# Optimization experiments

Measured on AMD Instinct MI355X. Metric: run time of the kernel, lower is better.

## Reference

```python
import jax, jax.numpy as jnp
import numpy as np

# Geometry constants (LinearProbeGeom)
N_DET = 128
N_T = 2048
DT_S = 2.5e-08        # 40 MHz sampling
PITCH_M = 3.0e-04
C_M_S = 1540.0
NX, NY = 256, 256
X0_M, DX_M = -0.0192, 1.5e-04
Y0_M, DY_M = 1.0e-03, 1.5e-04
ARRAY_X0_M, ARRAY_Y_M = -0.0192, 0.0
N_FFT = N_T  # fft_pad = 0
EPS = np.float32(np.finfo(np.float32).eps)


def _constants():
    freq = np.fft.rfftfreq(N_FFT, d=DT_S)
    omega = (2.0 * np.pi * freq).astype(np.float32)            # (F,)
    fw = np.ones_like(omega)
    if omega.size > 2:
        fw[1:-1] = 2.0
    if N_FFT % 2 == 0 and omega.size > 1:
        fw[-1] = 1.0
    kx = (2.0 * np.pi * np.fft.fftfreq(N_DET, d=PITCH_M)).astype(np.float32)  # (D,)
    xs = (X0_M + np.arange(NX) * DX_M - ARRAY_X0_M).astype(np.float32)        # (X,)
    ys = (Y0_M + np.arange(NY) * DY_M - ARRAY_Y_M).astype(np.float32)         # (Y,)
    # Hann apodization over detectors (buffer, non-trainable)
    apod = (0.5 - 0.5 * np.cos(2.0 * np.pi * np.arange(N_DET) / max(N_DET - 1, 1))).astype(np.float32)
    return (jnp.asarray(omega), jnp.asarray(fw), jnp.asarray(kx),
            jnp.asarray(xs), jnp.asarray(ys), jnp.asarray(apod))


def setup_inputs() -> dict:
    key = jax.random.key(0)
    sino = jax.random.normal(key, (8, 1, N_DET, N_T), dtype=jnp.float32)
    return {"sino": sino}


def reference(sino):
    omega, fw, kx, xs, ys, apod = _constants()
    B, C, D, T = sino.shape
    # per-(B,C) standardization over (det, time)
    mean = jnp.mean(sino, axis=(-1, -2), keepdims=True)
    sn = sino - mean
    var = jnp.mean(sn * sn, axis=(-1, -2), keepdims=True)
    sn = sn / jnp.sqrt(var + EPS)
    # time window is rectangular (window=None) -> identity
    sw = sn * apod[None, None, :, None]
    # 2D spectrum: rfft over time, fft over detectors
    spec = jnp.fft.rfft(sw, n=N_FFT, axis=-1)          # (B,C,D,F)
    spec = jnp.fft.fft(spec, axis=2)                   # (B,C,D,F)
    # Stolt dispersion: kz^2 = (w/c)^2 - kx^2, clamped
    kz_sq = (omega / C_M_S)[None, :] ** 2 - (kx ** 2)[:, None]   # (D,F)
    kz = jnp.sqrt(jnp.maximum(kz_sq, 0.0))
    prop_mask = (kz_sq > 0.0).astype(jnp.float32)
    # fold propagation mask and frequency weighting into the spectrum
    sf = spec * (prop_mask * fw[None, :])[None, None, :, :]      # (B,C,D,F) complex
    # per-depth phase shift and frequency reduction
    phase_y = jnp.exp(1j * kz[None, :, :] * ys[:, None, None])   # (Y,D,F) complex64
    band = jnp.einsum('bcdf,ydf->bcyd', sf, phase_y)             # (B,C,Y,D)
    # lateral inverse transform via explicit phase matrix
    phase_x = jnp.exp(1j * kx[:, None] * xs[None, :])            # (D,X)
    img = jnp.einsum('bcyd,dx->bcyx', band, phase_x)             # (B,C,Y,X)
    img_mag = jnp.abs(img)
    apod_sum = jnp.maximum(jnp.sum(apod), EPS)
    fw_sum = jnp.maximum(jnp.sum(fw), EPS)
    return img_mag / (apod_sum * fw_sum)
```

## Files before the change

kernel.cpp:

```cpp
#include <hip/hip_runtime.h>
#include <math.h>

#define NB 8
#define ND 128
#define NT 2048
#define NF 1025
#define NYY 256
#define NXX 256

#define SPEC_BYTES 8396800
#define BAND_PART_BYTES 2097152
#define BANDH_PART_BYTES 1048576
#define ROWSTAT_OFF 0
#define SPECT_OFF  8192
#define SF_OFF     (SPECT_OFF + SPEC_BYTES)
#define BAND_OFF   (SF_OFF + SPEC_BYTES)

__global__ __launch_bounds__(256) void fk_tfft(const float* __restrict__ sino,
                                               float2* __restrict__ specT,
                                               float2* __restrict__ rowstat) {
  const int row = blockIdx.x;
  const int d = row & (ND - 1);
  const int tid = threadIdx.x;
  __shared__ float2 bufA[1024];
  __shared__ float2 bufB[1024];
  __shared__ float2 wsum[4];
  const float ap = (float)(0.5 - 0.5 * cos(6.283185307179586 * (double)d / 127.0));
  const float2* in = (const float2*)(sino + (size_t)row * NT);
  float s = 0.f, q = 0.f;
  for (int i = tid; i < 1024; i += 256) {
    float2 v = in[i];
    s += v.x + v.y;
    q += v.x * v.x + v.y * v.y;
    bufA[i] = make_float2(v.x * ap, v.y * ap);
  }
  #pragma unroll
  for (int o = 32; o > 0; o >>= 1) {
    s += __shfl_down(s, o);
    q += __shfl_down(q, o);
  }
  if ((tid & 63) == 0) wsum[tid >> 6] = make_float2(s, q);
  __syncthreads();
  if (tid == 0) {
    rowstat[row] = make_float2(wsum[0].x + wsum[1].x + wsum[2].x + wsum[3].x,
                               wsum[0].y + wsum[1].y + wsum[2].y + wsum[3].y);
  }
  float2* src = bufA;
  float2* dst = bufB;
  for (int p = 1; p <= 512; p <<= 1) {
    #pragma unroll
    for (int it = 0; it < 2; ++it) {
      int i = tid + it * 256;
      int k = i & (p - 1);
      float2 u = src[i];
      float2 v = src[i + 512];
      float ang = -3.14159265358979323846f * ((float)k / (float)p);
      float sn, cs; __sincosf(ang, &sn, &cs);
      float2 vw = make_float2(v.x * cs - v.y * sn, v.x * sn + v.y * cs);
      int j = ((i - k) << 1) + k;
      dst[j]     = make_float2(u.x + vw.x, u.y + vw.y);
      dst[j + p] = make_float2(u.x - vw.x, u.y - vw.y);
    }
    __syncthreads();
    float2* t = src; src = dst; dst = t;
  }
  float2* out = specT + (size_t)row * NF;
  for (int k = tid; k < 1024; k += 256) {
    float2 zk = src[k];
    float2 zc = src[(1024 - k) & 1023]; zc.y = -zc.y;
    float2 xe = make_float2(0.5f * (zk.x + zc.x), 0.5f * (zk.y + zc.y));
    float ax = zk.x - zc.x, ay = zk.y - zc.y;
    float2 xo = make_float2(0.5f * ay, -0.5f * ax);
    float ang = -3.14159265358979323846f * ((float)k / 1024.0f);
    float sn, cs; __sincosf(ang, &sn, &cs);
    out[k] = make_float2(xe.x + cs * xo.x - sn * xo.y,
                         xe.y + cs * xo.y + sn * xo.x);
  }
  if (tid == 0) {
    float2 z0 = src[0];
    out[1024] = make_float2(z0.x - z0.y, 0.0f);
  }
}

__global__ __launch_bounds__(256) void fk_dfft(const float2* __restrict__ specT,
                                               float2* __restrict__ sf) {
  const int b = blockIdx.y;
  const int f0 = blockIdx.x * 4;
  const int sub = threadIdx.x >> 6;
  const int i = threadIdx.x & 63;
  const int f = f0 + sub;
  const bool valid = (f < NF);
  __shared__ float2 A[4][128];
  __shared__ float2 Bf[4][128];
  if (valid) {
    const float2* col = specT + ((size_t)b * ND) * NF + f;
    A[sub][i]      = col[(size_t)i * NF];
    A[sub][i + 64] = col[(size_t)(i + 64) * NF];
  }
  __syncthreads();
  float2 (*src)[128] = A;
  float2 (*dst)[128] = Bf;
  for (int p = 1; p <= 64; p <<= 1) {
    if (valid) {
      int k = i & (p - 1);
      float2 u = src[sub][i];
      float2 v = src[sub][i + 64];
      float ang = -3.14159265358979323846f * ((float)k / (float)p);
      float sn, cs; __sincosf(ang, &sn, &cs);
      float2 vw = make_float2(v.x * cs - v.y * sn, v.x * sn + v.y * cs);
      int j = ((i - k) << 1) + k;
      dst[sub][j]     = make_float2(u.x + vw.x, u.y + vw.y);
      dst[sub][j + p] = make_float2(u.x - vw.x, u.y - vw.y);
    }
    __syncthreads();
    float2 (*t)[128] = src; src = dst; dst = t;
  }
  if (valid) {
    const float fwv = (f == 0 || f == NF - 1) ? 1.0f : 2.0f;
    double freqd = (double)f / 5.12e-5;
    float omega = (float)(freqd * 6.283185307179586);
    float woc = omega / 1540.0f;
    float woc2 = __fmul_rn(woc, woc);
    #pragma unroll
    for (int h = 0; h < 2; ++h) {
      int kd = i + h * 64;
      int kt = kd < 64 ? kd : kd - 128;
      float kxv = (float)(6.283185307179586 * ((double)kt / 0.0384));
      float kzsq = __fsub_rn(woc2, __fmul_rn(kxv, kxv));
      float m = (kzsq > 0.0f) ? fwv : 0.0f;
      float2 v = src[sub][kd];
      sf[((size_t)(b * ND + kd)) * NF + f] = make_float2(v.x * m, v.y * m);
    }
  }
}

__device__ __forceinline__ unsigned int bf16rne(float x) {
  unsigned int u = __float_as_uint(x);
  return (u + 0x7fffu + ((u >> 16) & 1u)) >> 16;
}

__global__ __launch_bounds__(256, 3) void fk_band(const float2* __restrict__ sf,
                                                  unsigned int* __restrict__ bandh,
                                                  int flen_base, int fpad) {
  const int dblk = blockIdx.x;
  const int part = blockIdx.y;
  const int f0 = part * flen_base;
  const int flen = min(flen_base, NF - f0);
  const int tid = threadIdx.x;
  const int w = tid >> 6, l = tid & 63;
  const int d = dblk * 4 + w;

  extern __shared__ float lds[];
  float2* sfs = (float2*)lds;
  float4* kcs = (float4*)(lds + 64 * fpad);

  {
    const int row = tid >> 3;
    const int wr = row >> 3, br = row & 7;
    const int dr = dblk * 4 + wr;
    const float2* srcp = sf + ((size_t)(br * ND + dr)) * NF + f0;
    for (int ff = tid & 7; ff < fpad; ff += 8)
      sfs[row * fpad + ff] = (ff < flen) ? srcp[ff] : make_float2(0.f, 0.f);
  }
  for (int e = tid; e < 4 * fpad; e += 256) {
    const int wk = e / fpad, ff = e - wk * fpad;
    float kzv = 0.f;
    if (ff < flen) {
      int dk = dblk * 4 + wk;
      int kt = dk < 64 ? dk : dk - 128;
      float kxv = (float)(6.283185307179586 * ((double)kt / 0.0384));
      float kx2 = __fmul_rn(kxv, kxv);
      int f = f0 + ff;
      double freqd = (double)f / 5.12e-5;
      float omega = (float)(freqd * 6.283185307179586);
      float woc = omega / 1540.0f;
      float kzsq = __fsub_rn(__fmul_rn(woc, woc), kx2);
      kzv = (kzsq > 0.0f) ? sqrtf(kzsq) : 0.0f;
    }
    float sd, cd;
    __sincosf(kzv * 1.5e-4f, &sd, &cd);
    kcs[e] = make_float4(kzv, cd, sd, 0.f);
  }
  __syncthreads();

  const float y0 = (float)(1.0e-3 + (double)(4 * l) * 1.5e-4);

  float2 acc[8][4];
  #pragma unroll
  for (int b = 0; b < 8; ++b)
    #pragma unroll
    for (int i = 0; i < 4; ++i) acc[b][i] = make_float2(0.f, 0.f);

  const float4* kcw = kcs + w * fpad;
  const float2* rows = sfs + (w * 8) * fpad;

  #pragma unroll 2
  for (int ff = 0; ff < fpad; ++ff) {
    const float4 k4 = kcw[ff];
    float s0, c0;
    __sincosf(k4.x * y0, &s0, &c0);
    float2 ph[4];
    ph[0] = make_float2(c0, s0);
    #pragma unroll
    for (int i = 0; i < 3; ++i)
      ph[i + 1] = make_float2(ph[i].x * k4.y - ph[i].y * k4.z,
                              ph[i].x * k4.z + ph[i].y * k4.y);
    #pragma unroll
    for (int b = 0; b < 8; ++b) {
      float2 p = rows[b * fpad + ff];
      #pragma unroll
      for (int i = 0; i < 4; ++i) {
        acc[b][i].x = fmaf(p.x, ph[i].x, fmaf(-p.y, ph[i].y, acc[b][i].x));
        acc[b][i].y = fmaf(p.x, ph[i].y, fmaf( p.y, ph[i].x, acc[b][i].y));
      }
    }
  }

  unsigned int* outp = bandh + (size_t)part * (NB * ND * NYY);
  #pragma unroll
  for (int b = 0; b < 8; ++b) {
    uint4 pk;
    pk.x = bf16rne(acc[b][0].x) | (bf16rne(acc[b][0].y) << 16);
    pk.y = bf16rne(acc[b][1].x) | (bf16rne(acc[b][1].y) << 16);
    pk.z = bf16rne(acc[b][2].x) | (bf16rne(acc[b][2].y) << 16);
    pk.w = bf16rne(acc[b][3].x) | (bf16rne(acc[b][3].y) << 16);
    ((uint4*)(outp + ((size_t)(b * ND + d)) * NYY))[l] = pk;
  }
}

__global__ __launch_bounds__(256) void fk_sum(const unsigned int* __restrict__ bandh,
                                              float2* __restrict__ bandS, int nparts) {
  const int n = blockIdx.x * 256 + threadIdx.x;
  float sx = 0.f, sy = 0.f;
  for (int p = 0; p < nparts; ++p) {
    unsigned int u = bandh[(size_t)p * (NB * ND * NYY) + n];
    sx += __uint_as_float(u << 16);
    sy += __uint_as_float(u & 0xffff0000u);
  }
  bandS[n] = make_float2(sx, sy);
}

__global__ __launch_bounds__(256) void fk_img(const float2* __restrict__ bandS,
                                              const float2* __restrict__ rowstat,
                                              float* __restrict__ out, float inv_norm) {
  const int y = blockIdx.x;
  const int b = blockIdx.y;
  const int tid = threadIdx.x;
  __shared__ float2 A[256];
  __shared__ float2 Bb[256];
  __shared__ float2 spart[2];
  float2 myrs = make_float2(0.f, 0.f);
  if (tid < 128) myrs = rowstat[b * ND + tid];
  {
    float2 v = make_float2(0.f, 0.f);
    if (tid < 64)        v = bandS[((size_t)(b * ND + tid)) * NYY + y];
    else if (tid >= 192) v = bandS[((size_t)(b * ND + tid - 128)) * NYY + y];
    A[tid] = v;
  }
  {
    float s = myrs.x, q = myrs.y;
    #pragma unroll
    for (int o = 32; o > 0; o >>= 1) {
      s += __shfl_down(s, o);
      q += __shfl_down(q, o);
    }
    if (tid < 128 && (tid & 63) == 0) spart[tid >> 6] = make_float2(s, q);
  }
  __syncthreads();
  const float nInv = 1.0f / 262144.0f;
  float ssum = spart[0].x + spart[1].x;
  float qsum = spart[0].y + spart[1].y;
  float mean = ssum * nInv;
  float var = qsum * nInv - mean * mean;
  float scl = 1.0f / sqrtf(var + 1.1920928955078125e-7f);

  float2* src = A;
  float2* dst = Bb;
  for (int p = 1; p <= 128; p <<= 1) {
    if (tid < 128) {
      int i = tid;
      int k = i & (p - 1);
      float2 u = src[i];
      float2 v = src[i + 128];
      float ang = 3.14159265358979323846f * ((float)k / (float)p);
      float sn, cs; __sincosf(ang, &sn, &cs);
      float2 vw = make_float2(v.x * cs - v.y * sn, v.x * sn + v.y * cs);
      int j = ((i - k) << 1) + k;
      dst[j]     = make_float2(u.x + vw.x, u.y + vw.y);
      dst[j + p] = make_float2(u.x - vw.x, u.y - vw.y);
    }
    __syncthreads();
    float2* t = src; src = dst; dst = t;
  }
  float2 r = src[tid];
  float mag = sqrtf(r.x * r.x + r.y * r.y);
  out[((size_t)b * NYY + y) * NXX + tid] = mag * scl * inv_norm;
}

extern "C" void kernel_launch(void* const* d_in, const int* in_sizes, int n_in,
                              void* d_out, int out_size, void* d_ws, size_t ws_size,
                              hipStream_t stream) {
  const float* sino = (const float*)d_in[0];
  float* out = (float*)d_out;
  char* ws = (char*)d_ws;

  float2*       rowstat = (float2*)(ws + ROWSTAT_OFF);
  float2*       specT   = (float2*)(ws + SPECT_OFF);
  float2*       sf      = (float2*)(ws + SF_OFF);
  unsigned int* bandh   = (unsigned int*)(ws + BAND_OFF);

  int FPART = 8;
  if (ws_size >= (size_t)BAND_OFF + 24u * BANDH_PART_BYTES + BAND_PART_BYTES) FPART = 24;
  const int flen_base = (NF + FPART - 1) / FPART;
  const int fpad = (flen_base + 1) & ~1;
  const size_t band_lds = (size_t)fpad * 320;
  float2* bandS = (float2*)(ws + BAND_OFF + (size_t)FPART * BANDH_PART_BYTES);

  double apod_sum = 0.0;
  for (int n = 0; n < ND; ++n) apod_sum += 0.5 - 0.5 * cos(6.283185307179586 * (double)n / 127.0);
  const float inv_norm = (float)(1.0 / (apod_sum * 2048.0));

  fk_tfft<<<NB * ND, 256, 0, stream>>>(sino, specT, rowstat);
  fk_dfft<<<dim3((NF + 3) / 4, NB), 256, 0, stream>>>(specT, sf);
  fk_band<<<dim3(32, FPART), 256, band_lds, stream>>>(sf, bandh, flen_base, fpad);
  fk_sum <<<NB * ND * NYY / 256, 256, 0, stream>>>(bandh, bandS, FPART);
  fk_img <<<dim3(NYY, NB), 256, 0, stream>>>(bandS, rowstat, out, inv_norm);
}
```

Baseline: 76.65 us.

## Coalesce dfft column loads via LDS staging and pack band LDS as float4

fk_dfft now handles 8 frequencies per block. It first stages a (8 freq x 128 det) tile into shared memory with a loading pattern where adjacent threads read adjacent frequencies, then runs two 4-column FFT passes from that tile, so the strided per-column global loads become partially coalesced. fk_band repacks its shared-memory spectrum rows so each float4 holds two batches' complex values, halving the LDS loads in the inner loop. The trade-off is more shared memory and extra barriers in dfft, and the band kernel's LDS layout changes without changing the total LDS size.

```diff
diff --git a/kernel.cpp b/kernel.cpp
--- a/kernel.cpp
+++ b/kernel.cpp
@@ -85,23 +85,33 @@
 __global__ __launch_bounds__(256) void fk_dfft(const float2* __restrict__ specT,
                                                float2* __restrict__ sf) {
   const int b = blockIdx.y;
-  const int f0 = blockIdx.x * 4;
-  const int sub = threadIdx.x >> 6;
-  const int i = threadIdx.x & 63;
-  const int f = f0 + sub;
-  const bool valid = (f < NF);
+  const int f0 = blockIdx.x * 8;
+  const int tid = threadIdx.x;
+  __shared__ float2 T[8][128];
   __shared__ float2 A[4][128];
   __shared__ float2 Bf[4][128];
-  if (valid) {
-    const float2* col = specT + ((size_t)b * ND) * NF + f;
-    A[sub][i]      = col[(size_t)i * NF];
-    A[sub][i + 64] = col[(size_t)(i + 64) * NF];
+  {
+    const int fi = tid & 7, db = tid >> 3;
+    const int f = f0 + fi;
+    #pragma unroll
+    for (int pass = 0; pass < 4; ++pass) {
+      const int dd = db + pass * 32;
+      T[fi][dd] = (f < NF) ? specT[((size_t)(b * ND + dd)) * NF + f]
+                           : make_float2(0.f, 0.f);
+    }
   }
   __syncthreads();
-  float2 (*src)[128] = A;
-  float2 (*dst)[128] = Bf;
-  for (int p = 1; p <= 64; p <<= 1) {
-    if (valid) {
+  const int sub = tid >> 6;
+  const int i = tid & 63;
+  for (int g = 0; g < 2; ++g) {
+    const int f = f0 + g * 4 + sub;
+    const bool valid = (f < NF);
+    A[sub][i]      = T[g * 4 + sub][i];
+    A[sub][i + 64] = T[g * 4 + sub][i + 64];
+    __syncthreads();
+    float2 (*src)[128] = A;
+    float2 (*dst)[128] = Bf;
+    for (int p = 1; p <= 64; p <<= 1) {
       int k = i & (p - 1);
       float2 u = src[sub][i];
       float2 v = src[sub][i + 64];
@@ -111,26 +121,27 @@
       int j = ((i - k) << 1) + k;
       dst[sub][j]     = make_float2(u.x + vw.x, u.y + vw.y);
       dst[sub][j + p] = make_float2(u.x - vw.x, u.y - vw.y);
+      __syncthreads();
+      float2 (*t)[128] = src; src = dst; dst = t;
+    }
+    if (valid) {
+      const float fwv = (f == 0 || f == NF - 1) ? 1.0f : 2.0f;
+      double freqd = (double)f / 5.12e-5;
+      float omega = (float)(freqd * 6.283185307179586);
+      float woc = omega / 1540.0f;
+      float woc2 = __fmul_rn(woc, woc);
+      #pragma unroll
+      for (int h = 0; h < 2; ++h) {
+        int kd = i + h * 64;
+        int kt = kd < 64 ? kd : kd - 128;
+        float kxv = (float)(6.283185307179586 * ((double)kt / 0.0384));
+        float kzsq = __fsub_rn(woc2, __fmul_rn(kxv, kxv));
+        float m = (kzsq > 0.0f) ? fwv : 0.0f;
+        float2 v = src[sub][kd];
+        sf[((size_t)(b * ND + kd)) * NF + f] = make_float2(v.x * m, v.y * m);
+      }
     }
     __syncthreads();
-    float2 (*t)[128] = src; src = dst; dst = t;
-  }
-  if (valid) {
-    const float fwv = (f == 0 || f == NF - 1) ? 1.0f : 2.0f;
-    double freqd = (double)f / 5.12e-5;
-    float omega = (float)(freqd * 6.283185307179586);
-    float woc = omega / 1540.0f;
-    float woc2 = __fmul_rn(woc, woc);
-    #pragma unroll
-    for (int h = 0; h < 2; ++h) {
-      int kd = i + h * 64;
-      int kt = kd < 64 ? kd : kd - 128;
-      float kxv = (float)(6.283185307179586 * ((double)kt / 0.0384));
-      float kzsq = __fsub_rn(woc2, __fmul_rn(kxv, kxv));
-      float m = (kzsq > 0.0f) ? fwv : 0.0f;
-      float2 v = src[sub][kd];
-      sf[((size_t)(b * ND + kd)) * NF + f] = make_float2(v.x * m, v.y * m);
-    }
   }
 }
 
@@ -151,16 +162,25 @@
   const int d = dblk * 4 + w;
 
   extern __shared__ float lds[];
-  float2* sfs = (float2*)lds;
-  float4* kcs = (float4*)(lds + 64 * fpad);
+  float4* sfs4 = (float4*)lds;
+  float4* kcs  = (float4*)lds + 16 * fpad;
 
   {
-    const int row = tid >> 3;
-    const int wr = row >> 3, br = row & 7;
-    const int dr = dblk * 4 + wr;
-    const float2* srcp = sf + ((size_t)(br * ND + dr)) * NF + f0;
-    for (int ff = tid & 7; ff < fpad; ff += 8)
-      sfs[row * fpad + ff] = (ff < flen) ? srcp[ff] : make_float2(0.f, 0.f);
+    const int pr = tid >> 4;
+    const int w2 = pr >> 2;
+    const int j  = pr & 3;
+    const int dr = dblk * 4 + w2;
+    const float2* s0 = sf + ((size_t)((2 * j)     * ND + dr)) * NF + f0;
+    const float2* s1 = sf + ((size_t)((2 * j + 1) * ND + dr)) * NF + f0;
+    for (int ff = tid & 15; ff < fpad; ff += 16) {
+      float4 v = make_float4(0.f, 0.f, 0.f, 0.f);
+      if (ff < flen) {
+        float2 a = s0[ff];
+        float2 c = s1[ff];
+        v = make_float4(a.x, a.y, c.x, c.y);
+      }
+      sfs4[pr * fpad + ff] = v;
+    }
   }
   for (int e = tid; e < 4 * fpad; e += 256) {
     const int wk = e / fpad, ff = e - wk * fpad;
@@ -192,7 +212,7 @@
     for (int i = 0; i < 4; ++i) acc[b][i] = make_float2(0.f, 0.f);
 
   const float4* kcw = kcs + w * fpad;
-  const float2* rows = sfs + (w * 8) * fpad;
+  const float4* rows4 = sfs4 + (w * 4) * fpad;
 
   #pragma unroll 2
   for (int ff = 0; ff < fpad; ++ff) {
@@ -206,12 +226,14 @@
       ph[i + 1] = make_float2(ph[i].x * k4.y - ph[i].y * k4.z,
                               ph[i].x * k4.z + ph[i].y * k4.y);
     #pragma unroll
-    for (int b = 0; b < 8; ++b) {
-      float2 p = rows[b * fpad + ff];
+    for (int j = 0; j < 4; ++j) {
+      float4 p = rows4[j * fpad + ff];
       #pragma unroll
       for (int i = 0; i < 4; ++i) {
-        acc[b][i].x = fmaf(p.x, ph[i].x, fmaf(-p.y, ph[i].y, acc[b][i].x));
-        acc[b][i].y = fmaf(p.x, ph[i].y, fmaf( p.y, ph[i].x, acc[b][i].y));
+        acc[2*j][i].x   = fmaf(p.x, ph[i].x, fmaf(-p.y, ph[i].y, acc[2*j][i].x));
+        acc[2*j][i].y   = fmaf(p.x, ph[i].y, fmaf( p.y, ph[i].x, acc[2*j][i].y));
+        acc[2*j+1][i].x = fmaf(p.z, ph[i].x, fmaf(-p.w, ph[i].y, acc[2*j+1][i].x));
+        acc[2*j+1][i].y = fmaf(p.z, ph[i].y, fmaf( p.w, ph[i].x, acc[2*j+1][i].y));
       }
     }
   }
@@ -321,7 +343,7 @@
   const float inv_norm = (float)(1.0 / (apod_sum * 2048.0));
 
   fk_tfft<<<NB * ND, 256, 0, stream>>>(sino, specT, rowstat);
-  fk_dfft<<<dim3((NF + 3) / 4, NB), 256, 0, stream>>>(specT, sf);
+  fk_dfft<<<dim3((NF + 7) / 8, NB), 256, 0, stream>>>(specT, sf);
   fk_band<<<dim3(32, FPART), 256, band_lds, stream>>>(sf, bandh, flen_base, fpad);
   fk_sum <<<NB * ND * NYY / 256, 256, 0, stream>>>(bandh, bandS, FPART);
   fk_img <<<dim3(NYY, NB), 256, 0, stream>>>(bandS, rowstat, out, inv_norm);
```

Result: no change. 77.66 us (+1.3%).
